# Performance work log

Hardware: AMD Instinct MI355X
Metric: run time of the kernel (lower is better)

Reference implementation:

```python
import jax, jax.numpy as jnp
import numpy as np

B, T, C = 4, 1024, 1024
H, D = 16, 64


def setup_inputs() -> dict:
    key = jax.random.key(0)
    ks = jax.random.split(key, 5)
    sc = 0.02
    x = jax.random.normal(ks[0], (B, T, C), dtype=jnp.float32)
    Wq = jax.random.normal(ks[1], (H, C, D), dtype=jnp.float32) * sc
    Wk = jax.random.normal(ks[2], (H, C, D), dtype=jnp.float32) * sc
    Wv = jax.random.normal(ks[3], (H, C, D), dtype=jnp.float32) * sc
    Wp = jax.random.normal(ks[4], (H * D, C), dtype=jnp.float32) * sc
    bp = jnp.zeros((C,), dtype=jnp.float32)
    return {"x": x, "Wq": Wq, "Wk": Wk, "Wv": Wv, "Wp": Wp, "bp": bp}


def reference(x, Wq, Wk, Wv, Wp, bp):
    # per-head projections (bias-free, as in nanoGPT Head)
    q = jnp.einsum('btc,hcd->bhtd', x, Wq)
    k = jnp.einsum('btc,hcd->bhtd', x, Wk)
    v = jnp.einsum('btc,hcd->bhtd', x, Wv)
    scale = 1.0 / jnp.sqrt(jnp.asarray(D, dtype=x.dtype))
    scores = jnp.einsum('bhtd,bhsd->bhts', q, k) * scale  # [B,H,T,T]
    causal = jnp.tril(jnp.ones((T, T), dtype=bool))
    scores = jnp.where(causal, scores, jnp.asarray(-jnp.inf, dtype=scores.dtype))
    attn = jax.nn.softmax(scores, axis=-1)
    out = jnp.einsum('bhts,bhsd->bhtd', attn, v)  # [B,H,T,D]
    out = out.transpose(0, 2, 1, 3).reshape(B, T, H * D)  # concat heads
    return out @ Wp + bp  # final projection (dropout=0)
```

## Files before the change

### kernel.cpp

```cpp
#include <hip/hip_runtime.h>
#include <hip/hip_bf16.h>

typedef unsigned short u16;
typedef __bf16 bf16x8 __attribute__((ext_vector_type(8)));
typedef float floatx4 __attribute__((ext_vector_type(4)));

#define SB 4
#define ST 1024
#define SC 1024
#define SH 16
#define SD 64

__device__ __forceinline__ u16 f2bf(float f) {
    unsigned int u = __builtin_bit_cast(unsigned int, f);
    u += 0x7fffu + ((u >> 16) & 1u);
    return (u16)(u >> 16);
}

__device__ __forceinline__ void gload16(const u16* g, u16* l) {
    __builtin_amdgcn_global_load_lds(
        (const __attribute__((address_space(1))) unsigned int*)g,
        (__attribute__((address_space(3))) unsigned int*)l, 16, 0, 0);
}

__global__ void k_cvt_x(const float* __restrict__ x, u16* __restrict__ xb, int n4) {
    int i = blockIdx.x * blockDim.x + threadIdx.x;
    if (i < n4) {
        float4 v = ((const float4*)x)[i];
        uint2 o;
        o.x = (unsigned)f2bf(v.x) | ((unsigned)f2bf(v.y) << 16);
        o.y = (unsigned)f2bf(v.z) | ((unsigned)f2bf(v.w) << 16);
        ((uint2*)xb)[i] = o;
    }
}

__global__ void k_cvt_wqkv(const float* __restrict__ Wq, const float* __restrict__ Wk,
                           const float* __restrict__ Wv, u16* __restrict__ Wt) {
    __shared__ float tile[64][65];
    const int qkv = blockIdx.z, h = blockIdx.y, c0 = blockIdx.x * 64;
    const float* src = qkv == 0 ? Wq : (qkv == 1 ? Wk : Wv);
    #pragma unroll
    for (int i = 0; i < 16; ++i) {
        int idx = threadIdx.x + i * 256;
        int r = idx >> 6, d = idx & 63;
        tile[r][d] = src[(h * SC + c0 + r) * SD + d];
    }
    __syncthreads();
    #pragma unroll
    for (int i = 0; i < 16; ++i) {
        int idx = threadIdx.x + i * 256;
        int d = idx >> 6, cc = idx & 63;
        Wt[(qkv * 1024 + h * SD + d) * SC + c0 + cc] = f2bf(tile[cc][d]);
    }
}

__global__ void k_cvt_wp(const float* __restrict__ Wp, u16* __restrict__ Wt) {
    __shared__ float tile[64][65];
    const int n0 = blockIdx.x * 64, k0 = blockIdx.y * 64;
    #pragma unroll
    for (int i = 0; i < 16; ++i) {
        int idx = threadIdx.x + i * 256;
        int r = idx >> 6, nn = idx & 63;
        tile[r][nn] = Wp[(k0 + r) * SC + n0 + nn];
    }
    __syncthreads();
    #pragma unroll
    for (int i = 0; i < 16; ++i) {
        int idx = threadIdx.x + i * 256;
        int nr = idx >> 6, kk = idx & 63;
        Wt[(n0 + nr) * (SH * SD) + k0 + kk] = f2bf(tile[kk][nr]);
    }
}

__global__ void k_tv(const u16* __restrict__ V, u16* __restrict__ Vt) {
    __shared__ u16 tl[64 * 72];
    const int bh = blockIdx.y, t0 = blockIdx.x * 64;
    const int tid = threadIdx.x;
    #pragma unroll
    for (int i = 0; i < 2; ++i) {
        int idx = tid + i * 256;
        int r = idx >> 3, c = idx & 7;
        *(uint4*)&tl[r * 72 + c * 8] = *(const uint4*)&V[((long)bh * ST + t0 + r) * SD + c * 8];
    }
    __syncthreads();
    #pragma unroll
    for (int i = 0; i < 2; ++i) {
        int idx = tid + i * 256;
        int d = idx >> 3, tc = idx & 7;
        u16 tmp[8];
        #pragma unroll
        for (int e = 0; e < 8; ++e) tmp[e] = tl[(tc * 8 + e) * 72 + d];
        *(uint4*)&Vt[((long)bh * SD + d) * ST + t0 + tc * 8] = *(uint4*)tmp;
    }
}

template<int BM, int BN, int MODE>
__launch_bounds__(256)
__global__ void k_gemm(const u16* __restrict__ A, const u16* __restrict__ Bt,
                       int M, int N, int K,
                       u16* __restrict__ Qb, u16* __restrict__ Kb, u16* __restrict__ Vb,
                       const float* __restrict__ bias, float* __restrict__ Cout) {
    constexpr int SM = BM / 32, SN = BN / 32;
    __shared__ u16 Als[BM * 64];
    __shared__ u16 Bls[BN * 64];
    const int tid = threadIdx.x, lane = tid & 63, w = tid >> 6;
    const int quad = lane >> 4, l16 = lane & 15;
    const int sr = lane >> 3, sc = lane & 7;
    const int nt = N / BN;
    const int m0 = (blockIdx.x / nt) * BM, n0 = (blockIdx.x % nt) * BN;
    const int wm = (w >> 1) * (BM / 2), wn = (w & 1) * (BN / 2);

    floatx4 acc[SM][SN] = {};
    for (int k0 = 0; k0 < K; k0 += 64) {
        #pragma unroll
        for (int i = 0; i < BM / 32; ++i) {
            int rb = (w * (BM / 32) + i) * 8;
            gload16(&A[(long)(m0 + rb + sr) * K + k0 + ((sc ^ sr) << 3)], &Als[rb * 64]);
        }
        #pragma unroll
        for (int i = 0; i < BN / 32; ++i) {
            int rb = (w * (BN / 32) + i) * 8;
            gload16(&Bt[(long)(n0 + rb + sr) * K + k0 + ((sc ^ sr) << 3)], &Bls[rb * 64]);
        }
        __syncthreads();
        bf16x8 af[SM][2], bfr[SN][2];
        #pragma unroll
        for (int sm = 0; sm < SM; ++sm) {
            int row = wm + sm * 16 + l16;
            #pragma unroll
            for (int ks = 0; ks < 2; ++ks)
                af[sm][ks] = *(const bf16x8*)&Als[row * 64 + (((ks * 4 + quad) ^ (row & 7)) << 3)];
        }
        #pragma unroll
        for (int sn = 0; sn < SN; ++sn) {
            int row = wn + sn * 16 + l16;
            #pragma unroll
            for (int ks = 0; ks < 2; ++ks)
                bfr[sn][ks] = *(const bf16x8*)&Bls[row * 64 + (((ks * 4 + quad) ^ (row & 7)) << 3)];
        }
        #pragma unroll
        for (int ks = 0; ks < 2; ++ks)
            #pragma unroll
            for (int sm = 0; sm < SM; ++sm)
                #pragma unroll
                for (int sn = 0; sn < SN; ++sn)
                    acc[sm][sn] = __builtin_amdgcn_mfma_f32_16x16x32_bf16(bfr[sn][ks], af[sm][ks], acc[sm][sn], 0, 0, 0);
        __syncthreads();
    }
    if (MODE == 0) {
        const int qkv = n0 >> 10, h = (n0 & 1023) >> 6;
        u16* dst = qkv == 0 ? Qb : (qkv == 1 ? Kb : Vb);
        const float qs = qkv == 0 ? 0.18033688011112042f : 1.0f;
        #pragma unroll
        for (int sm = 0; sm < SM; ++sm) {
            const int m = m0 + wm + sm * 16 + l16;
            const long base = ((long)((m >> 10) * SH + h) * ST + (m & 1023)) << 6;
            #pragma unroll
            for (int sn = 0; sn < SN; ++sn) {
                const int d0 = (wn + sn * 16 + (quad << 2)) & 63;
                u16 pk[4];
                #pragma unroll
                for (int r = 0; r < 4; ++r) pk[r] = f2bf(acc[sm][sn][r] * qs);
                *(uint2*)&dst[base + d0] = *(uint2*)pk;
            }
        }
    } else {
        #pragma unroll
        for (int sn = 0; sn < SN; ++sn) {
            const int nb = n0 + wn + sn * 16 + (quad << 2);
            const float4 bv = *(const float4*)&bias[nb];
            #pragma unroll
            for (int sm = 0; sm < SM; ++sm) {
                const int m = m0 + wm + sm * 16 + l16;
                float4 o;
                o.x = acc[sm][sn][0] + bv.x;
                o.y = acc[sm][sn][1] + bv.y;
                o.z = acc[sm][sn][2] + bv.z;
                o.w = acc[sm][sn][3] + bv.w;
                *(float4*)&Cout[(long)m * N + nb] = o;
            }
        }
    }
}

__launch_bounds__(256)
__global__ void k_attn(const u16* __restrict__ Qg, const u16* __restrict__ Kg,
                       const u16* __restrict__ Vtg, u16* __restrict__ Og) {
    __shared__ u16 Kls[64 * 64];
    __shared__ u16 Vls[64 * 64];
    __shared__ u16 Pls[64 * 64];
    const int tid = threadIdx.x, lane = tid & 63, w = tid >> 6;
    const int quad = lane >> 4, l16 = lane & 15;
    const int sr = lane >> 3, sc = lane & 7;
    const int tile = 15 - (blockIdx.x >> 6);
    const int bh = blockIdx.x & 63;
    const int t0 = tile * 64;
    const int b = bh >> 4, h = bh & 15;
    const u16* Qbh = Qg + (long)bh * ST * SD;
    const u16* Kbh = Kg + (long)bh * ST * SD;
    const u16* Vbh = Vtg + (long)bh * SD * ST;

    bf16x8 qf[2];
    {
        const u16* qrow = Qbh + (t0 + w * 16 + l16) * SD;
        qf[0] = *(const bf16x8*)&qrow[quad * 8];
        qf[1] = *(const bf16x8*)&qrow[32 + quad * 8];
    }
    floatx4 oacc[4] = {};
    float lsum = 0.f;
    const int myt = t0 + w * 16 + l16;
    const int rowP = w * 16 + l16;

    for (int j = 0; j <= tile; ++j) {
        const int s0 = j * 64;
        #pragma unroll
        for (int i = 0; i < 2; ++i) {
            int rb = (w * 2 + i) * 8;
            gload16(&Kbh[(s0 + rb + sr) * SD + ((sc ^ sr) << 3)], &Kls[rb * 64]);
            gload16(&Vbh[(rb + sr) * ST + s0 + ((sc ^ sr) << 3)], &Vls[rb * 64]);
        }
        __syncthreads();

        floatx4 sa[4] = {};
        #pragma unroll
        for (int sn = 0; sn < 4; ++sn) {
            int row = sn * 16 + l16;
            #pragma unroll
            for (int ks = 0; ks < 2; ++ks) {
                bf16x8 kf = *(const bf16x8*)&Kls[row * 64 + (((ks * 4 + quad) ^ (row & 7)) << 3)];
                sa[sn] = __builtin_amdgcn_mfma_f32_16x16x32_bf16(kf, qf[ks], sa[sn], 0, 0, 0);
            }
        }
        const bool diag = (j == tile);
        #pragma unroll
        for (int sn = 0; sn < 4; ++sn) {
            const int sl = sn * 16 + (quad << 2);
            u16 pk[4];
            #pragma unroll
            for (int r = 0; r < 4; ++r) {
                float e = __builtin_exp2f(sa[sn][r]);
                if (diag && s0 + sl + r > myt) e = 0.f;
                lsum += e;
                pk[r] = (u16)(__builtin_bit_cast(unsigned int, e) >> 16);
            }
            *(uint2*)&Pls[rowP * 64 + ((((sl >> 3)) ^ (rowP & 7)) << 3) + ((quad & 1) << 2)] = *(uint2*)pk;
        }
        bf16x8 pf[2];
        #pragma unroll
        for (int ks = 0; ks < 2; ++ks)
            pf[ks] = *(const bf16x8*)&Pls[rowP * 64 + (((ks * 4 + quad) ^ (rowP & 7)) << 3)];
        #pragma unroll
        for (int dn = 0; dn < 4; ++dn) {
            int row = dn * 16 + l16;
            #pragma unroll
            for (int ks = 0; ks < 2; ++ks) {
                bf16x8 vf = *(const bf16x8*)&Vls[row * 64 + (((ks * 4 + quad) ^ (row & 7)) << 3)];
                oacc[dn] = __builtin_amdgcn_mfma_f32_16x16x32_bf16(vf, pf[ks], oacc[dn], 0, 0, 0);
            }
        }
        __syncthreads();
    }
    float l = lsum;
    l += __shfl_xor(l, 16);
    l += __shfl_xor(l, 32);
    const float inv = 1.0f / l;
    const long obase = ((long)(b * ST + myt) << 10) + h * SD;
    #pragma unroll
    for (int dn = 0; dn < 4; ++dn) {
        u16 pk[4];
        #pragma unroll
        for (int r = 0; r < 4; ++r) pk[r] = f2bf(oacc[dn][r] * inv);
        *(uint2*)&Og[obase + dn * 16 + (quad << 2)] = *(uint2*)pk;
    }
}

extern "C" void kernel_launch(void* const* d_in, const int* in_sizes, int n_in,
                              void* d_out, int out_size, void* d_ws, size_t ws_size,
                              hipStream_t stream) {
    const float* x  = (const float*)d_in[0];
    const float* Wq = (const float*)d_in[1];
    const float* Wk = (const float*)d_in[2];
    const float* Wv = (const float*)d_in[3];
    const float* Wp = (const float*)d_in[4];
    const float* bp = (const float*)d_in[5];
    float* out = (float*)d_out;

    char* ws = (char*)d_ws;
    u16* xb   = (u16*)(ws);
    u16* Wqkv = (u16*)(ws + (8ll  << 20));
    u16* Wpt  = (u16*)(ws + (14ll << 20));
    u16* Qb   = (u16*)(ws + (16ll << 20));
    u16* Kb   = (u16*)(ws + (24ll << 20));
    u16* Vb   = (u16*)(ws + (32ll << 20));
    u16* Ob   = (u16*)(ws + (40ll << 20));
    u16* Vt   = (u16*)(ws);

    k_cvt_x<<<4096, 256, 0, stream>>>(x, xb, SB * ST * SC / 4);
    k_cvt_wqkv<<<dim3(16, 16, 3), 256, 0, stream>>>(Wq, Wk, Wv, Wqkv);
    k_cvt_wp<<<dim3(16, 16), 256, 0, stream>>>(Wp, Wpt);
    k_gemm<128, 64, 0><<<32 * 48, 256, 0, stream>>>(xb, Wqkv, 4096, 3072, 1024, Qb, Kb, Vb, nullptr, nullptr);
    k_tv<<<dim3(16, 64), 256, 0, stream>>>(Vb, Vt);
    k_attn<<<1024, 256, 0, stream>>>(Qb, Kb, Vt, Ob);
    k_gemm<64, 64, 1><<<64 * 16, 256, 0, stream>>>(Ob, Wpt, 4096, 1024, 1024, nullptr, nullptr, nullptr, bp, out);
}
```

Before: 179.6 us.

## Fuse prep kernels, double-buffer GEMM and attention loads, write V transposed

Merges the three conversion kernels into one launch. Adds LDS double buffering with one barrier per iteration to both the GEMM and attention loops, so global-to-LDS loads for the next tile overlap compute on the current one. The QKV GEMM epilogue now writes V directly in transposed layout, which removes the separate transpose kernel but turns those stores into scattered 2-byte writes. The output projection GEMM moves from 64x64 to 128x64 tiles, halving its block count.

After: 164.2 us. 1.09x faster.

```diff
diff --git a/kernel.cpp b/kernel.cpp
--- a/kernel.cpp
+++ b/kernel.cpp
@@ -23,120 +23,105 @@
         (__attribute__((address_space(3))) unsigned int*)l, 16, 0, 0);
 }
 
-__global__ void k_cvt_x(const float* __restrict__ x, u16* __restrict__ xb, int n4) {
-    int i = blockIdx.x * blockDim.x + threadIdx.x;
-    if (i < n4) {
+__global__ void k_prep(const float* __restrict__ x,
+                       const float* __restrict__ Wq, const float* __restrict__ Wk,
+                       const float* __restrict__ Wv, const float* __restrict__ Wp,
+                       u16* __restrict__ xb, u16* __restrict__ Wqkv, u16* __restrict__ Wpt) {
+    __shared__ float tile[64 * 65];
+    const int id = blockIdx.x, tid = threadIdx.x;
+    if (id < 4096) {
+        int i = id * 256 + tid;
         float4 v = ((const float4*)x)[i];
         uint2 o;
         o.x = (unsigned)f2bf(v.x) | ((unsigned)f2bf(v.y) << 16);
         o.y = (unsigned)f2bf(v.z) | ((unsigned)f2bf(v.w) << 16);
         ((uint2*)xb)[i] = o;
-    }
-}
-
-__global__ void k_cvt_wqkv(const float* __restrict__ Wq, const float* __restrict__ Wk,
-                           const float* __restrict__ Wv, u16* __restrict__ Wt) {
-    __shared__ float tile[64][65];
-    const int qkv = blockIdx.z, h = blockIdx.y, c0 = blockIdx.x * 64;
-    const float* src = qkv == 0 ? Wq : (qkv == 1 ? Wk : Wv);
-    #pragma unroll
-    for (int i = 0; i < 16; ++i) {
-        int idx = threadIdx.x + i * 256;
-        int r = idx >> 6, d = idx & 63;
-        tile[r][d] = src[(h * SC + c0 + r) * SD + d];
-    }
-    __syncthreads();
-    #pragma unroll
-    for (int i = 0; i < 16; ++i) {
-        int idx = threadIdx.x + i * 256;
-        int d = idx >> 6, cc = idx & 63;
-        Wt[(qkv * 1024 + h * SD + d) * SC + c0 + cc] = f2bf(tile[cc][d]);
-    }
-}
-
-__global__ void k_cvt_wp(const float* __restrict__ Wp, u16* __restrict__ Wt) {
-    __shared__ float tile[64][65];
-    const int n0 = blockIdx.x * 64, k0 = blockIdx.y * 64;
-    #pragma unroll
-    for (int i = 0; i < 16; ++i) {
-        int idx = threadIdx.x + i * 256;
-        int r = idx >> 6, nn = idx & 63;
-        tile[r][nn] = Wp[(k0 + r) * SC + n0 + nn];
-    }
-    __syncthreads();
-    #pragma unroll
-    for (int i = 0; i < 16; ++i) {
-        int idx = threadIdx.x + i * 256;
-        int nr = idx >> 6, kk = idx & 63;
-        Wt[(n0 + nr) * (SH * SD) + k0 + kk] = f2bf(tile[kk][nr]);
-    }
-}
-
-__global__ void k_tv(const u16* __restrict__ V, u16* __restrict__ Vt) {
-    __shared__ u16 tl[64 * 72];
-    const int bh = blockIdx.y, t0 = blockIdx.x * 64;
-    const int tid = threadIdx.x;
-    #pragma unroll
-    for (int i = 0; i < 2; ++i) {
-        int idx = tid + i * 256;
-        int r = idx >> 3, c = idx & 7;
-        *(uint4*)&tl[r * 72 + c * 8] = *(const uint4*)&V[((long)bh * ST + t0 + r) * SD + c * 8];
-    }
-    __syncthreads();
-    #pragma unroll
-    for (int i = 0; i < 2; ++i) {
-        int idx = tid + i * 256;
-        int d = idx >> 3, tc = idx & 7;
-        u16 tmp[8];
-        #pragma unroll
-        for (int e = 0; e < 8; ++e) tmp[e] = tl[(tc * 8 + e) * 72 + d];
-        *(uint4*)&Vt[((long)bh * SD + d) * ST + t0 + tc * 8] = *(uint4*)tmp;
-    }
-}
-
-template<int BM, int BN, int MODE>
+    } else if (id < 4864) {
+        const int id1 = id - 4096;
+        const int qkv = id1 >> 8, rem = id1 & 255, h = rem >> 4, c0 = (rem & 15) * 64;
+        const float* src = qkv == 0 ? Wq : (qkv == 1 ? Wk : Wv);
+        #pragma unroll
+        for (int i = 0; i < 16; ++i) {
+            int idx = tid + i * 256;
+            int r = idx >> 6, d = idx & 63;
+            tile[r * 65 + d] = src[(h * SC + c0 + r) * SD + d];
+        }
+        __syncthreads();
+        #pragma unroll
+        for (int i = 0; i < 16; ++i) {
+            int idx = tid + i * 256;
+            int d = idx >> 6, cc = idx & 63;
+            Wqkv[(qkv * 1024 + h * SD + d) * SC + c0 + cc] = f2bf(tile[cc * 65 + d]);
+        }
+    } else {
+        const int id2 = id - 4864;
+        const int n0 = (id2 & 15) * 64, k0 = (id2 >> 4) * 64;
+        #pragma unroll
+        for (int i = 0; i < 16; ++i) {
+            int idx = tid + i * 256;
+            int r = idx >> 6, nn = idx & 63;
+            tile[r * 65 + nn] = Wp[(k0 + r) * SC + n0 + nn];
+        }
+        __syncthreads();
+        #pragma unroll
+        for (int i = 0; i < 16; ++i) {
+            int idx = tid + i * 256;
+            int nr = idx >> 6, kk = idx & 63;
+            Wpt[(n0 + nr) * (SH * SD) + k0 + kk] = f2bf(tile[kk * 65 + nr]);
+        }
+    }
+}
+
+template<int MODE>
 __launch_bounds__(256)
 __global__ void k_gemm(const u16* __restrict__ A, const u16* __restrict__ Bt,
                        int M, int N, int K,
-                       u16* __restrict__ Qb, u16* __restrict__ Kb, u16* __restrict__ Vb,
+                       u16* __restrict__ Qb, u16* __restrict__ Kb, u16* __restrict__ Vt,
                        const float* __restrict__ bias, float* __restrict__ Cout) {
-    constexpr int SM = BM / 32, SN = BN / 32;
-    __shared__ u16 Als[BM * 64];
-    __shared__ u16 Bls[BN * 64];
+    constexpr int BM = 128, BN = 64, SM = 4, SN = 2;
+    __shared__ u16 Als[2][BM * 64];
+    __shared__ u16 Bls[2][BN * 64];
     const int tid = threadIdx.x, lane = tid & 63, w = tid >> 6;
     const int quad = lane >> 4, l16 = lane & 15;
     const int sr = lane >> 3, sc = lane & 7;
     const int nt = N / BN;
     const int m0 = (blockIdx.x / nt) * BM, n0 = (blockIdx.x % nt) * BN;
-    const int wm = (w >> 1) * (BM / 2), wn = (w & 1) * (BN / 2);
+    const int wm = (w >> 1) * 64, wn = (w & 1) * 32;
+
+    auto stage = [&](int buf, int k0) {
+        #pragma unroll
+        for (int i = 0; i < 4; ++i) {
+            int rb = (w * 4 + i) * 8;
+            gload16(&A[(long)(m0 + rb + sr) * K + k0 + ((sc ^ sr) << 3)], &Als[buf][rb * 64]);
+        }
+        #pragma unroll
+        for (int i = 0; i < 2; ++i) {
+            int rb = (w * 2 + i) * 8;
+            gload16(&Bt[(long)(n0 + rb + sr) * K + k0 + ((sc ^ sr) << 3)], &Bls[buf][rb * 64]);
+        }
+    };
 
     floatx4 acc[SM][SN] = {};
-    for (int k0 = 0; k0 < K; k0 += 64) {
-        #pragma unroll
-        for (int i = 0; i < BM / 32; ++i) {
-            int rb = (w * (BM / 32) + i) * 8;
-            gload16(&A[(long)(m0 + rb + sr) * K + k0 + ((sc ^ sr) << 3)], &Als[rb * 64]);
-        }
-        #pragma unroll
-        for (int i = 0; i < BN / 32; ++i) {
-            int rb = (w * (BN / 32) + i) * 8;
-            gload16(&Bt[(long)(n0 + rb + sr) * K + k0 + ((sc ^ sr) << 3)], &Bls[rb * 64]);
-        }
-        __syncthreads();
+    const int niter = K / 64;
+    stage(0, 0);
+    for (int it = 0; it < niter; ++it) {
+        const int buf = it & 1;
+        __syncthreads();
+        if (it + 1 < niter) stage(buf ^ 1, (it + 1) * 64);
         bf16x8 af[SM][2], bfr[SN][2];
         #pragma unroll
         for (int sm = 0; sm < SM; ++sm) {
             int row = wm + sm * 16 + l16;
             #pragma unroll
             for (int ks = 0; ks < 2; ++ks)
-                af[sm][ks] = *(const bf16x8*)&Als[row * 64 + (((ks * 4 + quad) ^ (row & 7)) << 3)];
+                af[sm][ks] = *(const bf16x8*)&Als[buf][row * 64 + (((ks * 4 + quad) ^ (row & 7)) << 3)];
         }
         #pragma unroll
         for (int sn = 0; sn < SN; ++sn) {
             int row = wn + sn * 16 + l16;
             #pragma unroll
             for (int ks = 0; ks < 2; ++ks)
-                bfr[sn][ks] = *(const bf16x8*)&Bls[row * 64 + (((ks * 4 + quad) ^ (row & 7)) << 3)];
+                bfr[sn][ks] = *(const bf16x8*)&Bls[buf][row * 64 + (((ks * 4 + quad) ^ (row & 7)) << 3)];
         }
         #pragma unroll
         for (int ks = 0; ks < 2; ++ks)
@@ -145,23 +130,28 @@
                 #pragma unroll
                 for (int sn = 0; sn < SN; ++sn)
                     acc[sm][sn] = __builtin_amdgcn_mfma_f32_16x16x32_bf16(bfr[sn][ks], af[sm][ks], acc[sm][sn], 0, 0, 0);
-        __syncthreads();
     }
     if (MODE == 0) {
         const int qkv = n0 >> 10, h = (n0 & 1023) >> 6;
-        u16* dst = qkv == 0 ? Qb : (qkv == 1 ? Kb : Vb);
         const float qs = qkv == 0 ? 0.18033688011112042f : 1.0f;
         #pragma unroll
         for (int sm = 0; sm < SM; ++sm) {
             const int m = m0 + wm + sm * 16 + l16;
-            const long base = ((long)((m >> 10) * SH + h) * ST + (m & 1023)) << 6;
+            const int bb = m >> 10, t = m & 1023;
             #pragma unroll
             for (int sn = 0; sn < SN; ++sn) {
-                const int d0 = (wn + sn * 16 + (quad << 2)) & 63;
+                const int d0 = wn + sn * 16 + (quad << 2);
                 u16 pk[4];
                 #pragma unroll
                 for (int r = 0; r < 4; ++r) pk[r] = f2bf(acc[sm][sn][r] * qs);
-                *(uint2*)&dst[base + d0] = *(uint2*)pk;
+                if (qkv == 2) {
+                    const long vb = (long)(bb * SH + h) * SD * ST + t;
+                    #pragma unroll
+                    for (int r = 0; r < 4; ++r) Vt[vb + (long)(d0 + r) * ST] = pk[r];
+                } else {
+                    u16* dst = qkv == 0 ? Qb : Kb;
+                    *(uint2*)&dst[(((long)(bb * SH + h) * ST + t) << 6) + d0] = *(uint2*)pk;
+                }
             }
         }
     } else {
@@ -186,8 +176,8 @@
 __launch_bounds__(256)
 __global__ void k_attn(const u16* __restrict__ Qg, const u16* __restrict__ Kg,
                        const u16* __restrict__ Vtg, u16* __restrict__ Og) {
-    __shared__ u16 Kls[64 * 64];
-    __shared__ u16 Vls[64 * 64];
+    __shared__ u16 Kls[2][64 * 64];
+    __shared__ u16 Vls[2][64 * 64];
     __shared__ u16 Pls[64 * 64];
     const int tid = threadIdx.x, lane = tid & 63, w = tid >> 6;
     const int quad = lane >> 4, l16 = lane & 15;
@@ -211,15 +201,21 @@
     const int myt = t0 + w * 16 + l16;
     const int rowP = w * 16 + l16;
 
-    for (int j = 0; j <= tile; ++j) {
-        const int s0 = j * 64;
+    auto stage = [&](int buf, int s0) {
         #pragma unroll
         for (int i = 0; i < 2; ++i) {
             int rb = (w * 2 + i) * 8;
-            gload16(&Kbh[(s0 + rb + sr) * SD + ((sc ^ sr) << 3)], &Kls[rb * 64]);
-            gload16(&Vbh[(rb + sr) * ST + s0 + ((sc ^ sr) << 3)], &Vls[rb * 64]);
-        }
-        __syncthreads();
+            gload16(&Kbh[(s0 + rb + sr) * SD + ((sc ^ sr) << 3)], &Kls[buf][rb * 64]);
+            gload16(&Vbh[(rb + sr) * ST + s0 + ((sc ^ sr) << 3)], &Vls[buf][rb * 64]);
+        }
+    };
+
+    stage(0, 0);
+    for (int j = 0; j <= tile; ++j) {
+        const int buf = j & 1;
+        const int s0 = j * 64;
+        __syncthreads();
+        if (j < tile) stage(buf ^ 1, s0 + 64);
 
         floatx4 sa[4] = {};
         #pragma unroll
@@ -227,7 +223,7 @@
             int row = sn * 16 + l16;
             #pragma unroll
             for (int ks = 0; ks < 2; ++ks) {
-                bf16x8 kf = *(const bf16x8*)&Kls[row * 64 + (((ks * 4 + quad) ^ (row & 7)) << 3)];
+                bf16x8 kf = *(const bf16x8*)&Kls[buf][row * 64 + (((ks * 4 + quad) ^ (row & 7)) << 3)];
                 sa[sn] = __builtin_amdgcn_mfma_f32_16x16x32_bf16(kf, qf[ks], sa[sn], 0, 0, 0);
             }
         }
@@ -243,7 +239,7 @@
                 lsum += e;
                 pk[r] = (u16)(__builtin_bit_cast(unsigned int, e) >> 16);
             }
-            *(uint2*)&Pls[rowP * 64 + ((((sl >> 3)) ^ (rowP & 7)) << 3) + ((quad & 1) << 2)] = *(uint2*)pk;
+            *(uint2*)&Pls[rowP * 64 + (((sl >> 3) ^ (rowP & 7)) << 3) + ((quad & 1) << 2)] = *(uint2*)pk;
         }
         bf16x8 pf[2];
         #pragma unroll
@@ -254,11 +250,10 @@
             int row = dn * 16 + l16;
             #pragma unroll
             for (int ks = 0; ks < 2; ++ks) {
-                bf16x8 vf = *(const bf16x8*)&Vls[row * 64 + (((ks * 4 + quad) ^ (row & 7)) << 3)];
+                bf16x8 vf = *(const bf16x8*)&Vls[buf][row * 64 + (((ks * 4 + quad) ^ (row & 7)) << 3)];
                 oacc[dn] = __builtin_amdgcn_mfma_f32_16x16x32_bf16(vf, pf[ks], oacc[dn], 0, 0, 0);
             }
         }
-        __syncthreads();
     }
     float l = lsum;
     l += __shfl_xor(l, 16);
@@ -291,15 +286,11 @@
     u16* Wpt  = (u16*)(ws + (14ll << 20));
     u16* Qb   = (u16*)(ws + (16ll << 20));
     u16* Kb   = (u16*)(ws + (24ll << 20));
-    u16* Vb   = (u16*)(ws + (32ll << 20));
+    u16* Vt   = (u16*)(ws + (32ll << 20));
     u16* Ob   = (u16*)(ws + (40ll << 20));
-    u16* Vt   = (u16*)(ws);
-
-    k_cvt_x<<<4096, 256, 0, stream>>>(x, xb, SB * ST * SC / 4);
-    k_cvt_wqkv<<<dim3(16, 16, 3), 256, 0, stream>>>(Wq, Wk, Wv, Wqkv);
-    k_cvt_wp<<<dim3(16, 16), 256, 0, stream>>>(Wp, Wpt);
-    k_gemm<128, 64, 0><<<32 * 48, 256, 0, stream>>>(xb, Wqkv, 4096, 3072, 1024, Qb, Kb, Vb, nullptr, nullptr);
-    k_tv<<<dim3(16, 64), 256, 0, stream>>>(Vb, Vt);
+
+    k_prep<<<5120, 256, 0, stream>>>(x, Wq, Wk, Wv, Wp, xb, Wqkv, Wpt);
+    k_gemm<0><<<32 * 48, 256, 0, stream>>>(xb, Wqkv, 4096, 3072, 1024, Qb, Kb, Vt, nullptr, nullptr);
     k_attn<<<1024, 256, 0, stream>>>(Qb, Kb, Vt, Ob);
-    k_gemm<64, 64, 1><<<64 * 16, 256, 0, stream>>>(Ob, Wpt, 4096, 1024, 1024, nullptr, nullptr, nullptr, bp, out);
-}
+    k_gemm<1><<<32 * 16, 256, 0, stream>>>(Ob, Wpt, 4096, 1024, 1024, nullptr, nullptr, nullptr, bp, out);
+}
```
